# Kernel tuning notes

Hardware: AMD Instinct MI355X
Metric: run time of the kernel (lower is better)

## Reference

```python
import jax, jax.numpy as jnp
import numpy as np

B, S, D = 2, 2048, 2048
H, KVH = 32, 8
HD = D // H            # 64
G = H // KVH           # 4 query heads per kv head
CLIP = 8.0
THETA = 500000.0
EPS = 1e-6
SCALE = 1.0 / np.sqrt(HD)


def setup_inputs() -> dict:
    key = jax.random.key(0)
    ks = jax.random.split(key, 4)
    hidden_states = jax.random.normal(ks[0], (B, S, D), dtype=jnp.float32)
    attention_mask = jnp.ones((B, S), dtype=jnp.int32)
    position_ids = jnp.broadcast_to(jnp.arange(S, dtype=jnp.int32)[None, :], (B, S))
    causal_mask = jnp.tril(jnp.ones((S, S), dtype=bool))[None, None]
    std = 0.02
    w_qkv = jax.random.normal(ks[1], (D, D + 2 * KVH * HD), dtype=jnp.float32) * std
    w_out = jax.random.normal(ks[2], (D, D), dtype=jnp.float32) * std
    ln1_scale = jnp.ones((D,), dtype=jnp.float32)
    ln2_scale = jnp.ones((D,), dtype=jnp.float32)
    return {
        "hidden_states": hidden_states,
        "attention_mask": attention_mask,
        "position_ids": position_ids,
        "causal_mask": causal_mask,
        "ln1_scale": ln1_scale,
        "w_qkv": w_qkv,
        "w_out": w_out,
        "ln2_scale": ln2_scale,
    }


def _layernorm(x, scale):
    m = jnp.mean(x, axis=-1, keepdims=True)
    v = jnp.mean(jnp.square(x - m), axis=-1, keepdims=True)
    return (x - m) * jax.lax.rsqrt(v + EPS) * scale


def _rope(x, cos, sin):
    # neox style: rotate halves of head_dim. x: [B,S,h,HD], cos/sin: [B,S,1,HD/2]
    x1, x2 = jnp.split(x, 2, axis=-1)
    return jnp.concatenate([x1 * cos - x2 * sin, x2 * cos + x1 * sin], axis=-1)


def _forward(hidden_states, attention_mask, position_ids, causal_mask,
             ln1_scale, w_qkv, w_out, ln2_scale):
    residual = hidden_states
    x = _layernorm(hidden_states, ln1_scale)

    qkv = jnp.clip(x @ w_qkv, -CLIP, CLIP)  # [B,S,D+2*KVH*HD]
    q, kv = jnp.split(qkv, [D], axis=2)
    k, v = jnp.split(kv, [KVH * HD], axis=2)
    q = q.reshape(B, S, H, HD)
    k = k.reshape(B, S, KVH, HD)
    v = v.reshape(B, S, KVH, HD)

    inv_freq = 1.0 / (THETA ** (jnp.arange(0, HD, 2, dtype=jnp.float32) / HD))
    ang = position_ids.astype(jnp.float32)[..., None] * inv_freq  # [B,S,HD/2]
    cos = jnp.cos(ang)[:, :, None, :]
    sin = jnp.sin(ang)[:, :, None, :]
    q = _rope(q, cos, sin)
    k = _rope(k, cos, sin)

    # GQA: group query heads per kv head
    qg = q.reshape(B, S, KVH, G, HD)
    scores = jnp.einsum("bqhgd,bkhd->bhgqk", qg, k) * SCALE  # [B,KVH,G,S,S]
    mask = causal_mask[:, :, :S, :S] & (attention_mask[:, None, None, :] > 0)  # [B,1,S,S]
    bias = jnp.where(mask[:, :, None], 0.0, jnp.finfo(scores.dtype).min)
    probs = jax.nn.softmax(scores + bias, axis=-1)
    attn = jnp.einsum("bhgqk,bkhd->bqhgd", probs, v).reshape(B, S, D)

    attn_out = attn @ w_out
    hidden = attn_out + residual
    residual2 = hidden
    hidden = _layernorm(hidden, ln2_scale)
    return residual2, hidden


def reference(hidden_states, attention_mask, position_ids, causal_mask,
              ln1_scale, w_qkv, w_out, ln2_scale):
    return _forward(hidden_states, attention_mask, position_ids, causal_mask,
                    ln1_scale, w_qkv, w_out, ln2_scale)
```

## Files before the change

### kernel.cpp

```cpp
#include <hip/hip_runtime.h>
#include <hip/hip_bf16.h>
#include <stdint.h>

typedef __bf16 bf16_t;
typedef __bf16 bf16x8 __attribute__((ext_vector_type(8)));
typedef float f32x4 __attribute__((ext_vector_type(4)));
typedef _Float16 f16x8v __attribute__((ext_vector_type(8)));
typedef _Float16 f16x4v __attribute__((ext_vector_type(4)));

#define LOG2E 1.44269504088896f

__device__ __forceinline__ void load_lds16(const void* g, void* l) {
  __builtin_amdgcn_global_load_lds(
      (__attribute__((address_space(1))) unsigned int*)(uintptr_t)(g),
      (__attribute__((address_space(3))) unsigned int*)(l),
      16, 0, 0);
}

__device__ __forceinline__ f16x4v pack4_f16(float a, float b, float c, float d) {
  const __fp16 __attribute__((ext_vector_type(2))) lo = __builtin_amdgcn_cvt_pkrtz(a, b);
  const __fp16 __attribute__((ext_vector_type(2))) hi = __builtin_amdgcn_cvt_pkrtz(c, d);
  return __builtin_bit_cast(f16x4v, __builtin_shufflevector(lo, hi, 0, 1, 2, 3));
}

__global__ __launch_bounds__(256) void ln_kernel(
    const float* __restrict__ in, const float* __restrict__ gamma,
    bf16_t* __restrict__ out_bf, float* __restrict__ out_f)
{
  const int row = blockIdx.x;
  const int t = threadIdx.x;
  const float* x = in + (size_t)row * 2048;
  float4 a = ((const float4*)x)[t];
  float4 b = ((const float4*)x)[t + 256];
  float v[8] = {a.x, a.y, a.z, a.w, b.x, b.y, b.z, b.w};
  float s = 0.f, q = 0.f;
#pragma unroll
  for (int i = 0; i < 8; ++i) { s += v[i]; q += v[i] * v[i]; }
#pragma unroll
  for (int off = 1; off < 64; off <<= 1) {
    s += __shfl_xor(s, off, 64);
    q += __shfl_xor(q, off, 64);
  }
  __shared__ float red[4][2];
  if ((t & 63) == 0) { red[t >> 6][0] = s; red[t >> 6][1] = q; }
  __syncthreads();
  s = red[0][0] + red[1][0] + red[2][0] + red[3][0];
  q = red[0][1] + red[1][1] + red[2][1] + red[3][1];
  const float mean = s * (1.0f / 2048.0f);
  const float var = q * (1.0f / 2048.0f) - mean * mean;
  const float inv = rsqrtf(var + 1e-6f);
  float4 ga = ((const float4*)gamma)[t];
  float4 gb = ((const float4*)gamma)[t + 256];
  float g[8] = {ga.x, ga.y, ga.z, ga.w, gb.x, gb.y, gb.z, gb.w};
  float y[8];
#pragma unroll
  for (int i = 0; i < 8; ++i) y[i] = (v[i] - mean) * inv * g[i];
  if (out_bf) {
    alignas(16) bf16_t tb[8];
#pragma unroll
    for (int i = 0; i < 8; ++i) tb[i] = (bf16_t)y[i];
    bf16_t* o = out_bf + (size_t)row * 2048;
    *(uint2*)(o + t * 4) = *(const uint2*)(tb);
    *(uint2*)(o + (t + 256) * 4) = *(const uint2*)(tb + 4);
  } else {
    float* o = out_f + (size_t)row * 2048;
    ((float4*)o)[t] = make_float4(y[0], y[1], y[2], y[3]);
    ((float4*)o)[t + 256] = make_float4(y[4], y[5], y[6], y[7]);
  }
}

template <typename IT, typename OT>
__global__ __launch_bounds__(256) void transpose_cast(
    const IT* __restrict__ in, OT* __restrict__ out,
    int in_stride, int out_stride, long in_bstride, long out_bstride)
{
  const int bz = blockIdx.z;
  const IT* ib = in + (size_t)bz * in_bstride;
  OT* ob = out + (size_t)bz * out_bstride;
  const int c0 = blockIdx.x * 32, r0 = blockIdx.y * 32;
  const int tx = threadIdx.x, ty = threadIdx.y;
  __shared__ float tile[32][33];
#pragma unroll
  for (int i = 0; i < 4; ++i)
    tile[ty + i * 8][tx] = (float)ib[(size_t)(r0 + ty + i * 8) * in_stride + c0 + tx];
  __syncthreads();
#pragma unroll
  for (int i = 0; i < 4; ++i)
    ob[(size_t)(c0 + ty + i * 8) * out_stride + r0 + tx] = (OT)tile[tx][ty + i * 8];
}

__global__ __launch_bounds__(256) void gemm_bt(
    const bf16_t* __restrict__ A, const bf16_t* __restrict__ BT,
    int M, int N, int K, int mode,
    const float* __restrict__ resid, void* __restrict__ outv)
{
  __shared__ alignas(16) bf16_t As[128 * 32];
  __shared__ alignas(16) bf16_t Bs[128 * 32];
  const int t = threadIdx.x;
  const int lane = t & 63;
  const int wave = t >> 6;
  const int m0 = blockIdx.y * 128;
  const int n0 = blockIdx.x * 128;
  const int wm = (wave >> 1) * 64;
  const int wn = (wave & 1) * 64;

  f32x4 acc[4][4] = {};

  const int i0 = t, i1 = t + 256;
  const bf16_t* Ag0 = A + (size_t)(m0 + (i0 >> 2)) * K + (i0 & 3) * 8;
  const bf16_t* Ag1 = A + (size_t)(m0 + (i1 >> 2)) * K + (i1 & 3) * 8;
  const bf16_t* Bg0 = BT + (size_t)(n0 + (i0 >> 2)) * K + (i0 & 3) * 8;
  const bf16_t* Bg1 = BT + (size_t)(n0 + (i1 >> 2)) * K + (i1 & 3) * 8;
  bf16_t* AsW0 = As + (size_t)(wave * 64) * 8;
  bf16_t* AsW1 = As + (size_t)(256 + wave * 64) * 8;
  bf16_t* BsW0 = Bs + (size_t)(wave * 64) * 8;
  bf16_t* BsW1 = Bs + (size_t)(256 + wave * 64) * 8;

  const int rsel = lane & 15;
  const int ksel = (lane >> 4) * 8;

  for (int k0 = 0; k0 < K; k0 += 32) {
    __syncthreads();
    load_lds16(Ag0 + k0, AsW0);
    load_lds16(Ag1 + k0, AsW1);
    load_lds16(Bg0 + k0, BsW0);
    load_lds16(Bg1 + k0, BsW1);
    __syncthreads();
    bf16x8 af[4], bfr[4];
#pragma unroll
    for (int i = 0; i < 4; ++i) {
      af[i]  = *(const bf16x8*)(As + (wm + i * 16 + rsel) * 32 + ksel);
      bfr[i] = *(const bf16x8*)(Bs + (wn + i * 16 + rsel) * 32 + ksel);
    }
#pragma unroll
    for (int mi = 0; mi < 4; ++mi)
#pragma unroll
      for (int ni = 0; ni < 4; ++ni)
        acc[mi][ni] = __builtin_amdgcn_mfma_f32_16x16x32_bf16(af[mi], bfr[ni], acc[mi][ni], 0, 0, 0);
  }

  const int row_l = (lane >> 4) * 4;
  const int col_l = lane & 15;
#pragma unroll
  for (int mi = 0; mi < 4; ++mi) {
#pragma unroll
    for (int ni = 0; ni < 4; ++ni) {
      const size_t base = (size_t)(m0 + wm + mi * 16 + row_l) * N + (size_t)(n0 + wn + ni * 16 + col_l);
#pragma unroll
      for (int r = 0; r < 4; ++r) {
        float vv = acc[mi][ni][r];
        if (mode == 0) {
          vv = fminf(8.0f, fmaxf(-8.0f, vv));
          ((_Float16*)outv)[base + (size_t)r * N] = (_Float16)vv;
        } else {
          ((float*)outv)[base + (size_t)r * N] = vv + resid[base + (size_t)r * N];
        }
      }
    }
  }
}

__global__ __launch_bounds__(256) void rope_kernel(
    const _Float16* __restrict__ qkv, const int* __restrict__ pos_ids,
    _Float16* __restrict__ qo, _Float16* __restrict__ ko)
{
  const int bs = blockIdx.x;
  const int b = bs >> 11, s = bs & 2047;
  const float pos = (float)pos_ids[bs];
  const _Float16* row = qkv + (size_t)bs * 3072;
  const int t = threadIdx.x;
  const float qsc = 0.125f * LOG2E;
#pragma unroll
  for (int pp = 0; pp < 4; ++pp) {
    const int p = t + pp * 256;
    const int hh = p >> 5, i = p & 31;
    const float inv = exp2f(-0.59161151f * (float)i);
    float sn, cs;
    sincosf(pos * inv, &sn, &cs);
    const float x1 = (float)row[hh * 64 + i];
    const float x2 = (float)row[hh * 64 + 32 + i];
    _Float16* d = qo + (((size_t)b * 32 + hh) * 2048 + s) * 64 + i;
    d[0] = (_Float16)((x1 * cs - x2 * sn) * qsc);
    d[32] = (_Float16)((x2 * cs + x1 * sn) * qsc);
  }
  {
    const int p = t;
    const int hh = p >> 5, i = p & 31;
    const float inv = exp2f(-0.59161151f * (float)i);
    float sn, cs;
    sincosf(pos * inv, &sn, &cs);
    const float x1 = (float)row[2048 + hh * 64 + i];
    const float x2 = (float)row[2048 + hh * 64 + 32 + i];
    _Float16* d = ko + (((size_t)b * 8 + hh) * 2048 + s) * 64 + i;
    d[0] = (_Float16)(x1 * cs - x2 * sn);
    d[32] = (_Float16)(x2 * cs + x1 * sn);
  }
}

#define STAGE_TO(J, SI) do { \
    _Float16* d_ = &KV[(SI)][ksel][wv4]; \
    const _Float16* s_ = gsrc + (size_t)(J) * gstep; \
    load_lds16(s_, d_); \
    load_lds16(s_ + 32, d_ + 2048); \
  } while (0)

#define ABODY(J, BI, SI) do { \
    const int j_ = (J); \
    if (j_ == nit - 1) asm volatile("s_waitcnt vmcnt(0)" ::: "memory"); \
    else               asm volatile("s_waitcnt vmcnt(2)" ::: "memory"); \
    __builtin_amdgcn_s_barrier(); \
    __builtin_amdgcn_sched_barrier(0); \
    if (j_ + 2 < nit) STAGE_TO(j_ + 2, SI); \
    const _Float16* Kbuf = &KV[(BI)][0][0]; \
    const _Float16* Vbuf = &KV[(BI)][1][0]; \
    f32x4 st[4] = {}; \
    __builtin_amdgcn_s_setprio(1); \
    _Pragma("unroll") \
    for (int mt_ = 0; mt_ < 4; ++mt_) { \
      const f16x8v kf0_ = *(const f16x8v*)(Kbuf + krowc[mt_]); \
      const f16x8v kf1_ = *(const f16x8v*)(Kbuf + 2048 + krowc[mt_]); \
      st[mt_] = __builtin_amdgcn_mfma_f32_16x16x32_f16(kf0_, qf0, st[mt_], 0, 0, 0); \
      st[mt_] = __builtin_amdgcn_mfma_f32_16x16x32_f16(kf1_, qf1, st[mt_], 0, 0, 0); \
    } \
    __builtin_amdgcn_s_setprio(0); \
     \
    f16x4v vA_[4], vB_[4], vC_[4], vD_[4]; \
    _Pragma("unroll") \
    for (int nt_ = 0; nt_ < 4; ++nt_) { \
      const _Float16* Vr_ = Vbuf + vrow[nt_]; \
      vA_[nt_] = *(const f16x4v*)(Vr_ + vca); \
      vB_[nt_] = *(const f16x4v*)(Vr_ + vcb); \
      vC_[nt_] = *(const f16x4v*)(Vr_ + 2048 + vca); \
      vD_[nt_] = *(const f16x4v*)(Vr_ + 2048 + vcb); \
    } \
    const int k0_ = j_ * 64; \
    if (k0_ + 64 > q0) { \
      _Pragma("unroll") \
      for (int mt_ = 0; mt_ < 4; ++mt_) \
        _Pragma("unroll") \
        for (int r_ = 0; r_ < 4; ++r_) { \
          if (k0_ + mt_ * 16 + lg * 4 + r_ > myq) st[mt_][r_] = -3.0e38f; \
        } \
    } \
     \
    const float x0_ = fmaxf(fmaxf(st[0][0], st[0][1]), st[0][2]); \
    const float x1_ = fmaxf(fmaxf(st[0][3], st[1][0]), st[1][1]); \
    const float x2_ = fmaxf(fmaxf(st[1][2], st[1][3]), st[2][0]); \
    const float x3_ = fmaxf(fmaxf(st[2][1], st[2][2]), st[2][3]); \
    const float x4_ = fmaxf(fmaxf(st[3][0], st[3][1]), st[3][2]); \
    float mx_ = fmaxf(fmaxf(fmaxf(x0_, x1_), fmaxf(x2_, x3_)), fmaxf(x4_, st[3][3])); \
    if (__any(mx_ > m_r + 8.0f)) {   \
      mx_ = fmaxf(mx_, __shfl_xor(mx_, 16, 64)); \
      mx_ = fmaxf(mx_, __shfl_xor(mx_, 32, 64)); \
      const float mn_ = fmaxf(m_r, mx_); \
      const float al_ = exp2f(m_r - mn_); \
      _Pragma("unroll") \
      for (int r_ = 0; r_ < 4; ++r_) { \
        const float ao_ = __shfl(al_, lg * 4 + r_, 16); \
        ov[0][r_] *= ao_; ov[1][r_] *= ao_; ov[2][r_] *= ao_; ov[3][r_] *= ao_; \
        ovl[r_] *= ao_; \
      } \
      m_r = mn_; \
    } \
    f16x4v pf_[4]; \
    _Pragma("unroll") \
    for (int mt_ = 0; mt_ < 4; ++mt_) { \
      pf_[mt_] = pack4_f16(exp2f(st[mt_][0] - m_r), exp2f(st[mt_][1] - m_r), \
                           exp2f(st[mt_][2] - m_r), exp2f(st[mt_][3] - m_r)); \
    } \
    __builtin_amdgcn_s_setprio(1); \
    _Pragma("unroll") \
    for (int nt_ = 0; nt_ < 4; ++nt_) { \
      ov[nt_] = __builtin_amdgcn_mfma_f32_16x16x16f16(pf_[0], vA_[nt_], ov[nt_], 0, 0, 0); \
      ov[nt_] = __builtin_amdgcn_mfma_f32_16x16x16f16(pf_[1], vB_[nt_], ov[nt_], 0, 0, 0); \
      ov[nt_] = __builtin_amdgcn_mfma_f32_16x16x16f16(pf_[2], vC_[nt_], ov[nt_], 0, 0, 0); \
      ov[nt_] = __builtin_amdgcn_mfma_f32_16x16x16f16(pf_[3], vD_[nt_], ov[nt_], 0, 0, 0); \
    } \
    ovl = __builtin_amdgcn_mfma_f32_16x16x16f16(pf_[0], onesv, ovl, 0, 0, 0); \
    ovl = __builtin_amdgcn_mfma_f32_16x16x16f16(pf_[1], onesv, ovl, 0, 0, 0); \
    ovl = __builtin_amdgcn_mfma_f32_16x16x16f16(pf_[2], onesv, ovl, 0, 0, 0); \
    ovl = __builtin_amdgcn_mfma_f32_16x16x16f16(pf_[3], onesv, ovl, 0, 0, 0); \
    __builtin_amdgcn_s_setprio(0); \
  } while (0)

__global__ __launch_bounds__(512, 4) void attn_kernel(
    const _Float16* __restrict__ Q, const _Float16* __restrict__ Kb,
    const _Float16* __restrict__ Vt, bf16_t* __restrict__ Out)
{
  __shared__ alignas(16) _Float16 KV[3][2][4096];

  const int kvh = blockIdx.y;
  const int b = blockIdx.z;
  const int t = threadIdx.x;
  const int lane = t & 63;
  const int wave = t >> 6;
  const int g = wave >> 1;
  const int tile = wave & 1;
  const int h = kvh * 4 + g;
  const int ln15 = lane & 15;
  const int lg = lane >> 4;

  const _Float16* Qh = Q + ((size_t)(b * 32 + h) * 2048) * 64;
  const _Float16* Kh = Kb + ((size_t)(b * 8 + kvh) * 2048) * 64;
  const _Float16* Vh = Vt + ((size_t)(b * 8 + kvh) * 64) * 2048;

  const bool stK = (t < 256);
  const int u = t & 255;
  const int srow = u >> 2;
  const int scol = ((u & 3) ^ ((srow >> 1) & 3)) * 8;
  const _Float16* gsrc = stK ? (Kh + (size_t)srow * 64 + scol)
                             : (Vh + (size_t)srow * 2048 + scol);
  const int gstep = stK ? 64 * 64 : 64;
  const int ksel = stK ? 0 : 1;
  const int wv4 = (wave & 3) * 512;

  const int svz = (ln15 >> 1) & 3;
  const int kc = (lg ^ svz) * 8;
  const int vca = ((lg >> 1) ^ svz) * 8 + (lg & 1) * 4;
  const int vcb = (((lg >> 1) + 2) ^ svz) * 8 + (lg & 1) * 4;
  int krowc[4], vrow[4];
#pragma unroll
  for (int i = 0; i < 4; ++i) {
    krowc[i] = (i * 16 + ln15) * 32 + kc;
    vrow[i] = (i * 16 + ln15) * 32;
  }
  const f16x4v onesv = {(_Float16)1.0f, (_Float16)1.0f, (_Float16)1.0f, (_Float16)1.0f};

  for (int half = 0; half < 2; ++half) {
    const int qc = (half == 0) ? blockIdx.x : (63 - blockIdx.x);
    const int q0 = qc * 32 + tile * 16;
    const int myq = q0 + ln15;
    const int nit = (qc >> 1) + 1;

    const f16x8v qf0 = *(const f16x8v*)(Qh + (size_t)(q0 + ln15) * 64 + lg * 8);
    const f16x8v qf1 = *(const f16x8v*)(Qh + (size_t)(q0 + ln15) * 64 + 32 + lg * 8);

    f32x4 ov[4] = {};
    f32x4 ovl = {};
    float m_r = 0.0f;

    STAGE_TO(0, 0);
    if (nit > 1) STAGE_TO(1, 1);

    int it = 0;
    for (; it + 3 <= nit; it += 3) {
      ABODY(it, 0, 2);
      ABODY(it + 1, 1, 0);
      ABODY(it + 2, 2, 1);
    }
    if (it < nit) { ABODY(it, 0, 2); ++it; }
    if (it < nit) { ABODY(it, 1, 0); }

#pragma unroll
    for (int r = 0; r < 4; ++r) {
      const float ilo = 1.0f / ovl[r];
      const size_t obase = ((size_t)b * 2048 + (size_t)(q0 + lg * 4 + r)) * 2048 + (size_t)h * 64;
#pragma unroll
      for (int nt = 0; nt < 4; ++nt)
        Out[obase + nt * 16 + ln15] = (bf16_t)(ov[nt][r] * ilo);
    }
    __builtin_amdgcn_s_barrier();
    __builtin_amdgcn_sched_barrier(0);
  }
}
#undef ABODY
#undef STAGE_TO

extern "C" void kernel_launch(void* const* d_in, const int* in_sizes, int n_in,
                              void* d_out, int out_size, void* d_ws, size_t ws_size,
                              hipStream_t stream) {
  (void)in_sizes; (void)n_in; (void)out_size; (void)ws_size;
  const float* hid  = (const float*)d_in[0];
  const int*   pos  = (const int*)d_in[2];
  const float* ln1g = (const float*)d_in[4];
  const float* wqkv = (const float*)d_in[5];
  const float* wout = (const float*)d_in[6];
  const float* ln2g = (const float*)d_in[7];
  float* out = (float*)d_out;
  char* ws = (char*)d_ws;

  bf16_t*   xb  = (bf16_t*)(ws + 0);
  bf16_t*   wT  = (bf16_t*)(ws + 16777216);
  _Float16* qkv = (_Float16*)(ws + 29360128);
  _Float16* qb  = (_Float16*)(ws + 79691776);
  _Float16* kb  = (_Float16*)(ws + 96468992);
  _Float16* vt  = (_Float16*)(ws + 100663296);

  ln_kernel<<<4096, 256, 0, stream>>>(hid, ln1g, xb, nullptr);
  transpose_cast<float, bf16_t><<<dim3(96, 64, 1), dim3(32, 8), 0, stream>>>(wqkv, wT, 3072, 2048, 0, 0);
  gemm_bt<<<dim3(24, 32), 256, 0, stream>>>(xb, wT, 4096, 3072, 2048, 0, nullptr, qkv);
  rope_kernel<<<4096, 256, 0, stream>>>(qkv, pos, qb, kb);
  transpose_cast<_Float16, _Float16><<<dim3(16, 64, 2), dim3(32, 8), 0, stream>>>(
      qkv + 2560, vt, 3072, 2048, (long)2048 * 3072, (long)512 * 2048);
  transpose_cast<float, bf16_t><<<dim3(64, 64, 1), dim3(32, 8), 0, stream>>>(wout, wT, 2048, 2048, 0, 0);
  attn_kernel<<<dim3(32, 8, 2), 512, 0, stream>>>(qb, kb, vt, xb);
  gemm_bt<<<dim3(16, 32), 256, 0, stream>>>(xb, wT, 4096, 2048, 2048, 1, hid, out);
  ln_kernel<<<4096, 256, 0, stream>>>(out, ln2g, nullptr, out + 8388608);
}
```

Before: 372.9 us.

## Fuse RoPE into QKV GEMM epilogue and merge weight prep kernels

Removes the standalone rope kernel by applying the rotary embedding inside the QKV GEMM epilogue, writing Q and K directly in head-major layout using a precomputed cos/sin table. Both weight transposes and the sin/cos table generation are merged into one prep kernel launch, and the output-projection weights get their own buffer. This cuts two launches and one full read/write pass over the Q/K part of the qkv intermediate, at the cost of scattered per-row stores from the GEMM epilogue and a table lookup per element.

```diff
diff --git a/kernel.cpp b/kernel.cpp
--- a/kernel.cpp
+++ b/kernel.cpp
@@ -89,10 +89,45 @@
     ob[(size_t)(c0 + ty + i * 8) * out_stride + r0 + tx] = (OT)tile[tx][ty + i * 8];
 }
 
+__global__ __launch_bounds__(256) void prep_weights(
+    const float* __restrict__ wqkv, const float* __restrict__ wout,
+    bf16_t* __restrict__ qkvT, bf16_t* __restrict__ outT,
+    float2* __restrict__ tbl)
+{
+  const int bx = blockIdx.x, by = blockIdx.y, z = blockIdx.z;
+  const int tx = threadIdx.x, ty = threadIdx.y;
+  if (z == 1 && bx >= 64) {
+    const int flat = (bx - 64) * 64 + by;
+    if (flat < 256) {
+      const int idx = flat * 256 + ty * 32 + tx;
+      const int p = idx >> 5, i = idx & 31;
+      const float inv = exp2f(-0.59161151f * (float)i);
+      float sn, cs;
+      sincosf((float)p * inv, &sn, &cs);
+      tbl[idx] = make_float2(cs, sn);
+    }
+    return;
+  }
+  const float* in = z ? wout : wqkv;
+  bf16_t* out = z ? outT : qkvT;
+  const int in_stride = z ? 2048 : 3072;
+  const int c0 = bx * 32, r0 = by * 32;
+  __shared__ float tile[32][33];
+#pragma unroll
+  for (int i = 0; i < 4; ++i)
+    tile[ty + i * 8][tx] = in[(size_t)(r0 + ty + i * 8) * in_stride + c0 + tx];
+  __syncthreads();
+#pragma unroll
+  for (int i = 0; i < 4; ++i)
+    out[(size_t)(c0 + ty + i * 8) * 2048 + r0 + tx] = (bf16_t)tile[tx][ty + i * 8];
+}
+
 __global__ __launch_bounds__(256) void gemm_bt(
     const bf16_t* __restrict__ A, const bf16_t* __restrict__ BT,
     int M, int N, int K, int mode,
-    const float* __restrict__ resid, void* __restrict__ outv)
+    const float* __restrict__ resid, void* __restrict__ outv,
+    const int* __restrict__ pos, const float2* __restrict__ tbl,
+    _Float16* __restrict__ qo, _Float16* __restrict__ ko)
 {
   __shared__ alignas(16) bf16_t As[128 * 32];
   __shared__ alignas(16) bf16_t Bs[128 * 32];
@@ -141,59 +176,59 @@
 
   const int row_l = (lane >> 4) * 4;
   const int col_l = lane & 15;
-#pragma unroll
-  for (int mi = 0; mi < 4; ++mi) {
-#pragma unroll
-    for (int ni = 0; ni < 4; ++ni) {
-      const size_t base = (size_t)(m0 + wm + mi * 16 + row_l) * N + (size_t)(n0 + wn + ni * 16 + col_l);
-#pragma unroll
-      for (int r = 0; r < 4; ++r) {
-        float vv = acc[mi][ni][r];
-        if (mode == 0) {
-          vv = fminf(8.0f, fmaxf(-8.0f, vv));
-          ((_Float16*)outv)[base + (size_t)r * N] = (_Float16)vv;
-        } else {
-          ((float*)outv)[base + (size_t)r * N] = vv + resid[base + (size_t)r * N];
+  if (mode == 1) {
+#pragma unroll
+    for (int mi = 0; mi < 4; ++mi) {
+#pragma unroll
+      for (int ni = 0; ni < 4; ++ni) {
+        const size_t base = (size_t)(m0 + wm + mi * 16 + row_l) * N + (size_t)(n0 + wn + ni * 16 + col_l);
+#pragma unroll
+        for (int r = 0; r < 4; ++r)
+          ((float*)outv)[base + (size_t)r * N] = acc[mi][ni][r] + resid[base + (size_t)r * N];
+      }
+    }
+  } else {
+    const int headg = (n0 + wn) >> 6;
+    if (headg >= 40) {
+#pragma unroll
+      for (int mi = 0; mi < 4; ++mi) {
+#pragma unroll
+        for (int ni = 0; ni < 4; ++ni) {
+          const size_t base = (size_t)(m0 + wm + mi * 16 + row_l) * N + (size_t)(n0 + wn + ni * 16 + col_l);
+#pragma unroll
+          for (int r = 0; r < 4; ++r) {
+            const float vv = fminf(8.0f, fmaxf(-8.0f, acc[mi][ni][r]));
+            ((_Float16*)outv)[base + (size_t)r * N] = (_Float16)vv;
+          }
         }
       }
-    }
-  }
-}
-
-__global__ __launch_bounds__(256) void rope_kernel(
-    const _Float16* __restrict__ qkv, const int* __restrict__ pos_ids,
-    _Float16* __restrict__ qo, _Float16* __restrict__ ko)
-{
-  const int bs = blockIdx.x;
-  const int b = bs >> 11, s = bs & 2047;
-  const float pos = (float)pos_ids[bs];
-  const _Float16* row = qkv + (size_t)bs * 3072;
-  const int t = threadIdx.x;
-  const float qsc = 0.125f * LOG2E;
-#pragma unroll
-  for (int pp = 0; pp < 4; ++pp) {
-    const int p = t + pp * 256;
-    const int hh = p >> 5, i = p & 31;
-    const float inv = exp2f(-0.59161151f * (float)i);
-    float sn, cs;
-    sincosf(pos * inv, &sn, &cs);
-    const float x1 = (float)row[hh * 64 + i];
-    const float x2 = (float)row[hh * 64 + 32 + i];
-    _Float16* d = qo + (((size_t)b * 32 + hh) * 2048 + s) * 64 + i;
-    d[0] = (_Float16)((x1 * cs - x2 * sn) * qsc);
-    d[32] = (_Float16)((x2 * cs + x1 * sn) * qsc);
-  }
-  {
-    const int p = t;
-    const int hh = p >> 5, i = p & 31;
-    const float inv = exp2f(-0.59161151f * (float)i);
-    float sn, cs;
-    sincosf(pos * inv, &sn, &cs);
-    const float x1 = (float)row[2048 + hh * 64 + i];
-    const float x2 = (float)row[2048 + hh * 64 + 32 + i];
-    _Float16* d = ko + (((size_t)b * 8 + hh) * 2048 + s) * 64 + i;
-    d[0] = (_Float16)(x1 * cs - x2 * sn);
-    d[32] = (_Float16)(x2 * cs + x1 * sn);
+    } else {
+      const bool isq = headg < 32;
+      const int bb = m0 >> 11;
+      _Float16* hb = isq ? (qo + (size_t)(bb * 32 + headg) * 2048 * 64)
+                         : (ko + (size_t)(bb * 8 + (headg - 32)) * 2048 * 64);
+      const float sc = isq ? 0.125f * LOG2E : 1.0f;
+#pragma unroll
+      for (int mi = 0; mi < 4; ++mi) {
+#pragma unroll
+        for (int r = 0; r < 4; ++r) {
+          const int m = m0 + wm + mi * 16 + row_l + r;
+          const int s = m & 2047;
+          const int p = pos[m];
+          const float2* tp = tbl + (size_t)p * 32;
+          _Float16* drow = hb + (size_t)s * 64;
+#pragma unroll
+          for (int ni = 0; ni < 2; ++ni) {
+            const int i = ni * 16 + col_l;
+            const float2 cssn = tp[i];
+            const float x1 = (float)(_Float16)fminf(8.0f, fmaxf(-8.0f, acc[mi][ni][r]));
+            const float x2 = (float)(_Float16)fminf(8.0f, fmaxf(-8.0f, acc[mi][ni + 2][r]));
+            drow[i]      = (_Float16)((x1 * cssn.x - x2 * cssn.y) * sc);
+            drow[i + 32] = (_Float16)((x2 * cssn.x + x1 * cssn.y) * sc);
+          }
+        }
+      }
+    }
   }
 }
 
@@ -382,18 +417,20 @@
   bf16_t*   xb  = (bf16_t*)(ws + 0);
   bf16_t*   wT  = (bf16_t*)(ws + 16777216);
   _Float16* qkv = (_Float16*)(ws + 29360128);
+  float2*   tbl = (float2*)(ws + 54525952);
+  bf16_t*   wOT = (bf16_t*)(ws + 55050240);
   _Float16* qb  = (_Float16*)(ws + 79691776);
   _Float16* kb  = (_Float16*)(ws + 96468992);
   _Float16* vt  = (_Float16*)(ws + 100663296);
 
   ln_kernel<<<4096, 256, 0, stream>>>(hid, ln1g, xb, nullptr);
-  transpose_cast<float, bf16_t><<<dim3(96, 64, 1), dim3(32, 8), 0, stream>>>(wqkv, wT, 3072, 2048, 0, 0);
-  gemm_bt<<<dim3(24, 32), 256, 0, stream>>>(xb, wT, 4096, 3072, 2048, 0, nullptr, qkv);
-  rope_kernel<<<4096, 256, 0, stream>>>(qkv, pos, qb, kb);
+  prep_weights<<<dim3(96, 64, 2), dim3(32, 8), 0, stream>>>(wqkv, wout, wT, wOT, tbl);
+  gemm_bt<<<dim3(24, 32), 256, 0, stream>>>(xb, wT, 4096, 3072, 2048, 2, nullptr, qkv,
+                                            pos, tbl, qb, kb);
   transpose_cast<_Float16, _Float16><<<dim3(16, 64, 2), dim3(32, 8), 0, stream>>>(
       qkv + 2560, vt, 3072, 2048, (long)2048 * 3072, (long)512 * 2048);
-  transpose_cast<float, bf16_t><<<dim3(64, 64, 1), dim3(32, 8), 0, stream>>>(wout, wT, 2048, 2048, 0, 0);
   attn_kernel<<<dim3(32, 8, 2), 512, 0, stream>>>(qb, kb, vt, xb);
-  gemm_bt<<<dim3(16, 32), 256, 0, stream>>>(xb, wT, 4096, 2048, 2048, 1, hid, out);
+  gemm_bt<<<dim3(16, 32), 256, 0, stream>>>(xb, wOT, 4096, 2048, 2048, 1, hid, out,
+                                            nullptr, nullptr, nullptr, nullptr);
   ln_kernel<<<4096, 256, 0, stream>>>(out, ln2g, nullptr, out + 8388608);
 }
```

Result: slower. 384.0 us (+3.0%).

## Fuse pre-GEMM kernels and rope with V transpose; precompute rope sin/cos table

Applied to the files above, without the earlier changes.

Merges LN1, both weight transpose-casts and a rope cos/sin table build into one launch, and merges rope with the V transpose into a second launch. This cuts launch count and per-element sincos work. The out-projection weight now gets its own buffer, so it is transposed early instead of overwriting wT. Costs are branchy, heterogeneous blocks and an extra table read per rope element.

```diff
diff --git a/kernel.cpp b/kernel.cpp
--- a/kernel.cpp
+++ b/kernel.cpp
@@ -69,24 +69,126 @@
   }
 }
 
-template <typename IT, typename OT>
-__global__ __launch_bounds__(256) void transpose_cast(
-    const IT* __restrict__ in, OT* __restrict__ out,
-    int in_stride, int out_stride, long in_bstride, long out_bstride)
+__global__ __launch_bounds__(256) void fused_pre(
+    const float* __restrict__ hid, const float* __restrict__ ln1g,
+    bf16_t* __restrict__ xb,
+    const float* __restrict__ wqkv, const float* __restrict__ wout,
+    bf16_t* __restrict__ wT, bf16_t* __restrict__ wOT,
+    float2* __restrict__ tbl)
 {
-  const int bz = blockIdx.z;
-  const IT* ib = in + (size_t)bz * in_bstride;
-  OT* ob = out + (size_t)bz * out_bstride;
-  const int c0 = blockIdx.x * 32, r0 = blockIdx.y * 32;
-  const int tx = threadIdx.x, ty = threadIdx.y;
+  const int bid = blockIdx.x;
+  const int t = threadIdx.x;
+  if (bid < 4096) {
+    const float* x = hid + (size_t)bid * 2048;
+    float4 a = ((const float4*)x)[t];
+    float4 b = ((const float4*)x)[t + 256];
+    float v[8] = {a.x, a.y, a.z, a.w, b.x, b.y, b.z, b.w};
+    float s = 0.f, q = 0.f;
+#pragma unroll
+    for (int i = 0; i < 8; ++i) { s += v[i]; q += v[i] * v[i]; }
+#pragma unroll
+    for (int off = 1; off < 64; off <<= 1) {
+      s += __shfl_xor(s, off, 64);
+      q += __shfl_xor(q, off, 64);
+    }
+    __shared__ float red[4][2];
+    if ((t & 63) == 0) { red[t >> 6][0] = s; red[t >> 6][1] = q; }
+    __syncthreads();
+    s = red[0][0] + red[1][0] + red[2][0] + red[3][0];
+    q = red[0][1] + red[1][1] + red[2][1] + red[3][1];
+    const float mean = s * (1.0f / 2048.0f);
+    const float var = q * (1.0f / 2048.0f) - mean * mean;
+    const float inv = rsqrtf(var + 1e-6f);
+    float4 ga = ((const float4*)ln1g)[t];
+    float4 gb = ((const float4*)ln1g)[t + 256];
+    float g[8] = {ga.x, ga.y, ga.z, ga.w, gb.x, gb.y, gb.z, gb.w};
+    alignas(16) bf16_t tb[8];
+#pragma unroll
+    for (int i = 0; i < 8; ++i) tb[i] = (bf16_t)((v[i] - mean) * inv * g[i]);
+    bf16_t* o = xb + (size_t)bid * 2048;
+    *(uint2*)(o + t * 4) = *(const uint2*)(tb);
+    *(uint2*)(o + (t + 256) * 4) = *(const uint2*)(tb + 4);
+    return;
+  }
+  if (bid >= 14336) {
+    const int idx = (bid - 14336) * 256 + t;
+    const int p = idx >> 5, i = idx & 31;
+    const float inv = exp2f(-0.59161151f * (float)i);
+    float sn, cs;
+    sincosf((float)p * inv, &sn, &cs);
+    tbl[idx] = make_float2(cs, sn);
+    return;
+  }
+  const bool isQ = bid < 10240;
+  const int i6 = isQ ? (bid - 4096) : (bid - 10240);
+  const int bx = isQ ? (i6 % 96) : (i6 & 63);
+  const int by = isQ ? (i6 / 96) : (i6 >> 6);
+  const float* in = isQ ? wqkv : wout;
+  bf16_t* out = isQ ? wT : wOT;
+  const int in_stride = isQ ? 3072 : 2048;
+  const int c0 = bx * 32, r0 = by * 32;
+  const int tx = t & 31, ty = t >> 5;
   __shared__ float tile[32][33];
 #pragma unroll
   for (int i = 0; i < 4; ++i)
-    tile[ty + i * 8][tx] = (float)ib[(size_t)(r0 + ty + i * 8) * in_stride + c0 + tx];
+    tile[ty + i * 8][tx] = in[(size_t)(r0 + ty + i * 8) * in_stride + c0 + tx];
   __syncthreads();
 #pragma unroll
   for (int i = 0; i < 4; ++i)
-    ob[(size_t)(c0 + ty + i * 8) * out_stride + r0 + tx] = (OT)tile[tx][ty + i * 8];
+    out[(size_t)(c0 + ty + i * 8) * 2048 + r0 + tx] = (bf16_t)tile[tx][ty + i * 8];
+}
+
+__global__ __launch_bounds__(256) void rope_v(
+    const _Float16* __restrict__ qkv, const int* __restrict__ pos_ids,
+    const float2* __restrict__ tbl,
+    _Float16* __restrict__ qo, _Float16* __restrict__ ko,
+    _Float16* __restrict__ vt)
+{
+  const int bid = blockIdx.x;
+  const int t = threadIdx.x;
+  __shared__ float tile[32][33];
+  if (bid < 4096) {
+    const int b = bid >> 11, s = bid & 2047;
+    const float2* tp = tbl + (size_t)pos_ids[bid] * 32;
+    const _Float16* row = qkv + (size_t)bid * 3072;
+    const float qsc = 0.125f * LOG2E;
+#pragma unroll
+    for (int pp = 0; pp < 4; ++pp) {
+      const int p = t + pp * 256;
+      const int hh = p >> 5, i = p & 31;
+      const float2 cssn = tp[i];
+      const float x1 = (float)row[hh * 64 + i];
+      const float x2 = (float)row[hh * 64 + 32 + i];
+      _Float16* d = qo + (((size_t)b * 32 + hh) * 2048 + s) * 64 + i;
+      d[0] = (_Float16)((x1 * cssn.x - x2 * cssn.y) * qsc);
+      d[32] = (_Float16)((x2 * cssn.x + x1 * cssn.y) * qsc);
+    }
+    {
+      const int hh = t >> 5, i = t & 31;
+      const float2 cssn = tp[i];
+      const float x1 = (float)row[2048 + hh * 64 + i];
+      const float x2 = (float)row[2048 + hh * 64 + 32 + i];
+      _Float16* d = ko + (((size_t)b * 8 + hh) * 2048 + s) * 64 + i;
+      d[0] = (_Float16)(x1 * cssn.x - x2 * cssn.y);
+      d[32] = (_Float16)(x2 * cssn.x + x1 * cssn.y);
+    }
+    return;
+  }
+  const int idx = bid - 4096;
+  const int bz = idx >> 10;
+  const int rem = idx & 1023;
+  const int bx = rem & 15, by = rem >> 4;
+  const _Float16* ib = qkv + 2560 + (size_t)bz * 2048 * 3072;
+  _Float16* ob = vt + (size_t)bz * 512 * 2048;
+  const int c0 = bx * 32, r0 = by * 32;
+  const int tx = t & 31, ty = t >> 5;
+#pragma unroll
+  for (int i = 0; i < 4; ++i)
+    tile[ty + i * 8][tx] = (float)ib[(size_t)(r0 + ty + i * 8) * 3072 + c0 + tx];
+  __syncthreads();
+#pragma unroll
+  for (int i = 0; i < 4; ++i)
+    ob[(size_t)(c0 + ty + i * 8) * 2048 + r0 + tx] = (_Float16)tile[tx][ty + i * 8];
 }
 
 __global__ __launch_bounds__(256) void gemm_bt(
@@ -157,43 +259,6 @@
         }
       }
     }
-  }
-}
-
-__global__ __launch_bounds__(256) void rope_kernel(
-    const _Float16* __restrict__ qkv, const int* __restrict__ pos_ids,
-    _Float16* __restrict__ qo, _Float16* __restrict__ ko)
-{
-  const int bs = blockIdx.x;
-  const int b = bs >> 11, s = bs & 2047;
-  const float pos = (float)pos_ids[bs];
-  const _Float16* row = qkv + (size_t)bs * 3072;
-  const int t = threadIdx.x;
-  const float qsc = 0.125f * LOG2E;
-#pragma unroll
-  for (int pp = 0; pp < 4; ++pp) {
-    const int p = t + pp * 256;
-    const int hh = p >> 5, i = p & 31;
-    const float inv = exp2f(-0.59161151f * (float)i);
-    float sn, cs;
-    sincosf(pos * inv, &sn, &cs);
-    const float x1 = (float)row[hh * 64 + i];
-    const float x2 = (float)row[hh * 64 + 32 + i];
-    _Float16* d = qo + (((size_t)b * 32 + hh) * 2048 + s) * 64 + i;
-    d[0] = (_Float16)((x1 * cs - x2 * sn) * qsc);
-    d[32] = (_Float16)((x2 * cs + x1 * sn) * qsc);
-  }
-  {
-    const int p = t;
-    const int hh = p >> 5, i = p & 31;
-    const float inv = exp2f(-0.59161151f * (float)i);
-    float sn, cs;
-    sincosf(pos * inv, &sn, &cs);
-    const float x1 = (float)row[2048 + hh * 64 + i];
-    const float x2 = (float)row[2048 + hh * 64 + 32 + i];
-    _Float16* d = ko + (((size_t)b * 8 + hh) * 2048 + s) * 64 + i;
-    d[0] = (_Float16)(x1 * cs - x2 * sn);
-    d[32] = (_Float16)(x2 * cs + x1 * sn);
   }
 }
 
@@ -382,18 +447,16 @@
   bf16_t*   xb  = (bf16_t*)(ws + 0);
   bf16_t*   wT  = (bf16_t*)(ws + 16777216);
   _Float16* qkv = (_Float16*)(ws + 29360128);
+  float2*   tbl = (float2*)(ws + 54525952);
+  bf16_t*   wOT = (bf16_t*)(ws + 55050240);
   _Float16* qb  = (_Float16*)(ws + 79691776);
   _Float16* kb  = (_Float16*)(ws + 96468992);
   _Float16* vt  = (_Float16*)(ws + 100663296);
 
-  ln_kernel<<<4096, 256, 0, stream>>>(hid, ln1g, xb, nullptr);
-  transpose_cast<float, bf16_t><<<dim3(96, 64, 1), dim3(32, 8), 0, stream>>>(wqkv, wT, 3072, 2048, 0, 0);
+  fused_pre<<<14592, 256, 0, stream>>>(hid, ln1g, xb, wqkv, wout, wT, wOT, tbl);
   gemm_bt<<<dim3(24, 32), 256, 0, stream>>>(xb, wT, 4096, 3072, 2048, 0, nullptr, qkv);
-  rope_kernel<<<4096, 256, 0, stream>>>(qkv, pos, qb, kb);
-  transpose_cast<_Float16, _Float16><<<dim3(16, 64, 2), dim3(32, 8), 0, stream>>>(
-      qkv + 2560, vt, 3072, 2048, (long)2048 * 3072, (long)512 * 2048);
-  transpose_cast<float, bf16_t><<<dim3(64, 64, 1), dim3(32, 8), 0, stream>>>(wout, wT, 2048, 2048, 0, 0);
+  rope_v<<<6144, 256, 0, stream>>>(qkv, pos, tbl, qb, kb, vt);
   attn_kernel<<<dim3(32, 8, 2), 512, 0, stream>>>(qb, kb, vt, xb);
-  gemm_bt<<<dim3(16, 32), 256, 0, stream>>>(xb, wT, 4096, 2048, 2048, 1, hid, out);
+  gemm_bt<<<dim3(16, 32), 256, 0, stream>>>(xb, wOT, 4096, 2048, 2048, 1, hid, out);
   ln_kernel<<<4096, 256, 0, stream>>>(out, ln2g, nullptr, out + 8388608);
 }
```

Result: no change. 374.6 us (+0.5%).
